# Optimization experiments

Hardware: AMD Instinct MI355X
Metric: run time of the kernel (lower is better)

Reference implementation:

```python
import jax, jax.numpy as jnp
import numpy as np

B, H, IN, OUT, T = 1024, 1024, 512, 8192, 15
EPS = 1e-5


def setup_inputs() -> dict:
    key = jax.random.key(0)
    ks = jax.random.split(key, 20)
    s = 0.02
    d = {
        'z': jax.random.normal(ks[0], (B, H), jnp.float32),
        'input_length': T,
        # ConvTranspose1d weights, torch layout [in, out, k] == jax 'IOH'
        'cw1': jax.random.normal(ks[1], (H, H, 3), jnp.float32) * s,
        'cb1': jax.random.normal(ks[2], (H,), jnp.float32) * s,
        'cw2': jax.random.normal(ks[3], (H, H, 3), jnp.float32) * s,
        'cb2': jax.random.normal(ks[4], (H,), jnp.float32) * s,
        'cw3': jax.random.normal(ks[5], (H, H, 3), jnp.float32) * s,
        'cb3': jax.random.normal(ks[6], (H,), jnp.float32) * s,
        # BatchNorm1d (eval mode: running stats)
        'bn1_g': jnp.ones((H,), jnp.float32), 'bn1_b': jnp.zeros((H,), jnp.float32),
        'bn1_m': jax.random.normal(ks[7], (H,), jnp.float32) * 0.1,
        'bn1_v': jax.random.uniform(ks[8], (H,), jnp.float32, 0.5, 1.5),
        'bn2_g': jnp.ones((H,), jnp.float32), 'bn2_b': jnp.zeros((H,), jnp.float32),
        'bn2_m': jax.random.normal(ks[9], (H,), jnp.float32) * 0.1,
        'bn2_v': jax.random.uniform(ks[10], (H,), jnp.float32, 0.5, 1.5),
        # GRUCell: weight_ih [3H, IN+H], weight_hh [3H, H]
        'w_ih': jax.random.normal(ks[11], (3 * H, IN + H), jnp.float32) * s,
        'w_hh': jax.random.normal(ks[12], (3 * H, H), jnp.float32) * s,
        'b_ih': jax.random.normal(ks[13], (3 * H,), jnp.float32) * s,
        'b_hh': jax.random.normal(ks[14], (3 * H,), jnp.float32) * s,
        # Linears (torch layout [out_features, in_features])
        'h2x_w': jax.random.normal(ks[15], (IN, H), jnp.float32) * s,
        'h2x_b': jax.random.normal(ks[16], (IN,), jnp.float32) * s,
        'dec2out_w': jax.random.normal(ks[17], (OUT, H), jnp.float32) * s,
        'dec2out_b': jnp.zeros((OUT,), jnp.float32),
        'out_w': jax.random.normal(ks[18], (OUT, H), jnp.float32) * s,
        'out_b': jnp.zeros((OUT,), jnp.float32),
    }
    return d


def _conv_t(x, w, b):
    # x: [B, C, L] ; torch ConvTranspose1d(k=3, s=2, pad=0): out L -> 2L+1
    y = jax.lax.conv_transpose(x, w, strides=(2,), padding='VALID',
                               dimension_numbers=('NCH', 'IOH', 'NCH'),
                               transpose_kernel=True)
    return y + b[None, :, None]


def _bn(x, g, bta, m, v):
    inv = g / jnp.sqrt(v + EPS)
    return (x - m[None, :, None]) * inv[None, :, None] + bta[None, :, None]


def reference(z, input_length, cw1, cb1, cw2, cb2, cw3, cb3,
              bn1_g, bn1_b, bn1_m, bn1_v, bn2_g, bn2_b, bn2_m, bn2_v,
              w_ih, w_hh, b_ih, b_hh, h2x_w, h2x_b,
              dec2out_w, dec2out_b, out_w, out_b):
    b = z.shape[0]
    # conv-transpose context: [B, H, 1] -> [B, H, 15]
    dec = z[:, :, None]
    dec = _bn(jax.nn.elu(_conv_t(dec, cw1, cb1)), bn1_g, bn1_b, bn1_m, bn1_v)
    dec = _bn(jax.nn.elu(_conv_t(dec, cw2, cb2)), bn2_g, bn2_b, bn2_m, bn2_v)
    dec = _conv_t(dec, cw3, cb3)
    dec_tbh = jnp.transpose(dec, (2, 0, 1))[:input_length]  # [T, B, H]

    inp0 = jnp.full((b, IN), float(OUT - 2), z.dtype)

    def step(carry, dec_t):
        h, inp = carry
        x = jnp.concatenate([inp, dec_t], axis=1)         # [B, IN+H]
        gi = x @ w_ih.T + b_ih
        gh = h @ w_hh.T + b_hh
        ir, iz, inn = jnp.split(gi, 3, axis=1)
        hr, hz, hn = jnp.split(gh, 3, axis=1)
        r = jax.nn.sigmoid(ir + hr)
        zg = jax.nn.sigmoid(iz + hz)
        n = jnp.tanh(inn + r * hn)
        h_new = (1.0 - zg) * n + zg * h
        inp_new = jax.nn.relu(h_new @ h2x_w.T + h2x_b)    # eval-mode branch
        return (h_new, inp_new), h_new

    (_, _), hs = jax.lax.scan(step, (z, inp0), dec_tbh)   # hs: [T, B, H]

    dec_flat = dec_tbh.reshape(-1, H)
    out_flat = hs.reshape(-1, H)
    dec_o = dec_flat @ dec2out_w.T + dec2out_b            # [T*B, OUT]
    output = out_flat @ out_w.T + out_b                   # [T*B, OUT]
    return output, dec_o
```

## Files before the change

kernel.cpp:

```cpp
#include <hip/hip_runtime.h>
#include <math.h>


#define HD    1024
#define BATCH 1024
#define IND   512
#define OUTD  8192
#define TSTEPS 15
#define EPSV  1e-5f

typedef unsigned short u16;
typedef __attribute__((ext_vector_type(8))) short bf16x8;
typedef __attribute__((ext_vector_type(8))) unsigned short u16x8;
typedef __attribute__((ext_vector_type(4))) unsigned short u16x4;
typedef __attribute__((ext_vector_type(4))) float f32x4;

__device__ __forceinline__ u16 f2b(float f) {
    union { float f; unsigned u; } x; x.f = f;
    unsigned r = x.u + 0x7fffu + ((x.u >> 16) & 1u);
    return (u16)(r >> 16);
}
__device__ __forceinline__ float b2f(u16 v) {
    union { unsigned u; float f; } x; x.u = ((unsigned)v) << 16; return x.f;
}

typedef __attribute__((address_space(1))) const void gas_t;
typedef __attribute__((address_space(3))) void las_t;
__device__ __forceinline__ void gload_lds16(const u16* g, u16* l) {
    __builtin_amdgcn_global_load_lds((gas_t*)g, (las_t*)l, 16, 0, 0);
}

template<int OUTB>
__launch_bounds__(512, 2)
__global__ void gemm256(int nbn, int nk,
    const u16* __restrict__ A, const u16* __restrict__ B,
    const float* __restrict__ bias, float* __restrict__ Cf,
    u16* __restrict__ Cb, int lda, int ldb, int ldc)
{
    const int nwg = gridDim.x;
    const int q = nwg >> 3, r = nwg & 7;
    const int xcd = blockIdx.x & 7, idx = blockIdx.x >> 3;
    const int wg = (xcd < r ? xcd * (q + 1) : r * (q + 1) + (xcd - r) * q) + idx;
    const int bm = (wg / nbn) * 256;
    const int bn = (wg % nbn) * 256;

    __shared__ __align__(16) u16 smem[2][2][256 * 64];
    u16 (*As)[256 * 64] = smem[0];
    u16 (*Bs)[256 * 64] = smem[1];

    const int tid = threadIdx.x;
    const int w = tid >> 6, l = tid & 63;
    const int wr = w >> 2, wc = w & 3;
    const int srow = l >> 3;
    const int scb  = (l & 7) ^ srow;
    const int fr = l & 15, fcb = l >> 4, swz = l & 7;

    const u16* Ag = A + (size_t)bm * lda;
    const u16* Bg = B + (size_t)bn * ldb;

    auto stage = [&](int b, int kt) {
        const int k0 = kt * 64 + scb * 8;
#pragma unroll
        for (int rr = 0; rr < 4; ++rr)
            gload_lds16(Ag + (size_t)(rr * 64 + w * 8 + srow) * lda + k0,
                        &As[b][(rr * 64 + w * 8) * 64]);
#pragma unroll
        for (int rr = 0; rr < 4; ++rr)
            gload_lds16(Bg + (size_t)(rr * 64 + w * 8 + srow) * ldb + k0,
                        &Bs[b][(rr * 64 + w * 8) * 64]);
    };

    f32x4 acc[8][4];
#pragma unroll
    for (int m = 0; m < 8; ++m)
#pragma unroll
        for (int n = 0; n < 4; ++n) acc[m][n] = (f32x4){0.f, 0.f, 0.f, 0.f};

    stage(0, 0);
    asm volatile("s_waitcnt vmcnt(0)" ::: "memory");
    asm volatile("s_barrier" ::: "memory");

    for (int kt = 0; kt < nk; ++kt) {
        const int c = kt & 1;
        if (kt + 1 < nk) stage(c ^ 1, kt + 1);
#pragma unroll
        for (int ks = 0; ks < 2; ++ks) {
            bf16x8 av[8], bv[4];
#pragma unroll
            for (int m = 0; m < 8; ++m)
                av[m] = *(const bf16x8*)&As[c][
                    (wr * 128 + m * 16 + fr) * 64 + (((ks * 4 + fcb) ^ swz) * 8)];
#pragma unroll
            for (int n = 0; n < 4; ++n)
                bv[n] = *(const bf16x8*)&Bs[c][
                    (wc * 64 + n * 16 + fr) * 64 + (((ks * 4 + fcb) ^ swz) * 8)];
            __builtin_amdgcn_s_setprio(1);
#pragma unroll
            for (int m = 0; m < 8; ++m)
#pragma unroll
                for (int n = 0; n < 4; ++n)
                    acc[m][n] = __builtin_amdgcn_mfma_f32_16x16x32_bf16(
                                    av[m], bv[n], acc[m][n], 0, 0, 0);
            __builtin_amdgcn_s_setprio(0);
        }
        asm volatile("s_waitcnt vmcnt(0)" ::: "memory");
        asm volatile("s_barrier" ::: "memory");
    }

    float* fsm = (float*)smem;
    const int row_h = (l >> 4) * 4;
#pragma unroll 1
    for (int hh = 0; hh < 2; ++hh) {
        __syncthreads();
        if (wr == hh) {
#pragma unroll
            for (int m = 0; m < 8; ++m)
#pragma unroll
                for (int j = 0; j < 4; ++j) {
                    const int rl = m * 16 + row_h + j;
#pragma unroll
                    for (int n = 0; n < 4; ++n)
                        fsm[rl * 256 + wc * 64 + n * 16 + fr] = acc[m][n][j];
                }
        }
        __syncthreads();
#pragma unroll
        for (int it = 0; it < 16; ++it) {
            const int fid = it * 512 + tid;
            const int rl = fid >> 6;
            const int cf = (fid & 63) * 4;
            float4 v = *(const float4*)&fsm[rl * 256 + cf];
            v.x += bias[bn + cf + 0];
            v.y += bias[bn + cf + 1];
            v.z += bias[bn + cf + 2];
            v.w += bias[bn + cf + 3];
            if (OUTB) {
                u16x4 o;
                o[0] = f2b(v.x); o[1] = f2b(v.y); o[2] = f2b(v.z); o[3] = f2b(v.w);
                *(u16x4*)&Cb[(size_t)(bm + hh * 128 + rl) * ldc + bn + cf] = o;
            } else {
                *(float4*)&Cf[(size_t)(bm + hh * 128 + rl) * ldc + bn + cf] = v;
            }
        }
    }
}

template<int EPI>
__device__ __forceinline__ void gemm_tile(
    int bm, int bn,
    int K1, const u16* A1, int lda1, const u16* B1, int ldb1,
    int K2, const u16* A2, int lda2, const u16* B2, int ldb2,
    const float* bias,
    const float* bng, const float* bnb, const float* bnm, const float* bnv,
    u16* Cb, int ldc)
{
    __shared__ __align__(16) u16 As[128 * 32];
    __shared__ __align__(16) u16 Bs[128 * 32];

    const int tid  = threadIdx.x;
    const int lane = tid & 63;
    const int w    = tid >> 6;
    const int wr   = w >> 1, wc = w & 1;
    const int r_in = lane >> 2;
    const int c_in = (lane & 3) * 8;

    f32x4 acc[4][4];
#pragma unroll
    for (int m = 0; m < 4; ++m)
#pragma unroll
        for (int n = 0; n < 4; ++n) acc[m][n] = (f32x4){0.f, 0.f, 0.f, 0.f};

#pragma unroll 1
    for (int pair = 0; pair < 2; ++pair) {
        const int K = pair ? K2 : K1;
        if (K == 0) continue;
        const int lda = pair ? lda2 : lda1;
        const int ldb = pair ? ldb2 : ldb1;
        const u16* Ag = (pair ? A2 : A1) + (size_t)bm * lda;
        const u16* Bg = (pair ? B2 : B1) + (size_t)bn * ldb;

        for (int k0 = 0; k0 < K; k0 += 32) {
#pragma unroll
            for (int i = 0; i < 2; ++i) {
                gload_lds16(Ag + (size_t)(i * 64 + w * 16 + r_in) * lda + k0 + c_in,
                            &As[i * 2048 + w * 512]);
                gload_lds16(Bg + (size_t)(i * 64 + w * 16 + r_in) * ldb + k0 + c_in,
                            &Bs[i * 2048 + w * 512]);
            }
            __syncthreads();

            const int fr = lane & 15;
            const int fk = (lane >> 4) * 8;
            bf16x8 av[4], bv[4];
#pragma unroll
            for (int m = 0; m < 4; ++m)
                av[m] = *(const bf16x8*)&As[(wr * 64 + m * 16 + fr) * 32 + fk];
#pragma unroll
            for (int n = 0; n < 4; ++n)
                bv[n] = *(const bf16x8*)&Bs[(wc * 64 + n * 16 + fr) * 32 + fk];
#pragma unroll
            for (int m = 0; m < 4; ++m)
#pragma unroll
                for (int n = 0; n < 4; ++n)
                    acc[m][n] = __builtin_amdgcn_mfma_f32_16x16x32_bf16(
                                    av[m], bv[n], acc[m][n], 0, 0, 0);
            __syncthreads();
        }
    }

    const int col_l = lane & 15;
    const int row_h = (lane >> 4) * 4;
#pragma unroll
    for (int m = 0; m < 4; ++m) {
#pragma unroll
        for (int j = 0; j < 4; ++j) {
            const int row = bm + wr * 64 + m * 16 + row_h + j;
#pragma unroll
            for (int n = 0; n < 4; ++n) {
                const int col = bn + wc * 64 + n * 16 + col_l;
                float v = acc[m][n][j] + bias[col];
                if (EPI == 1) {
                    float e = v > 0.f ? v : expm1f(v);
                    float sc = bng[col] * rsqrtf(bnv[col] + EPSV);
                    v = (e - bnm[col]) * sc + bnb[col];
                }
                Cb[(size_t)row * ldc + col] = f2b(v);
            }
        }
    }
}

template<int EPI>
__launch_bounds__(256)
__global__ void conv_gemm(int Lin, const u16* X, const u16* W, const float* bias,
                          const float* bng, const float* bnb, const float* bnm, const float* bnv,
                          u16* Y)
{
    const int t = blockIdx.z;
    int l0 = 0, k0 = 0, l1 = 0, k1 = 0, cnt = 0;
    for (int l = 0; l < Lin; ++l) {
        int k = t - 2 * l;
        if (k >= 0 && k < 3) { if (!cnt) { l0 = l; k0 = k; } else { l1 = l; k1 = k; } ++cnt; }
    }
    const size_t BH = (size_t)BATCH * HD, HH = (size_t)HD * HD;
    gemm_tile<EPI>(blockIdx.y * 128, blockIdx.x * 128,
        HD, X + l0 * BH, HD, W + k0 * HH, HD,
        cnt > 1 ? HD : 0, X + l1 * BH, HD, W + k1 * HH, HD,
        bias, bng, bnb, bnm, bnv, Y + (size_t)t * BH, HD);
}

#define KTILE(Ag, lda_, Bg, ldb_, k0_, ACC2)                                      \
  {                                                                               \
    const int k0 = (k0_);                                                         \
    gload_lds16((Ag) + (size_t)(tid >> 2) * (lda_) + k0 + (tid & 3) * 8,          \
                &As[tid * 8]);                                                    \
    _Pragma("unroll")                                                             \
    for (int i_ = 0; i_ < 3; ++i_) {                                              \
      const int u_ = tid + i_ * 256;                                              \
      gload_lds16((Bg) + (size_t)((u_ >> 8) * HD + bn + ((u_ & 255) >> 2)) * (ldb_)\
                       + k0 + (u_ & 3) * 8,                                       \
                  &Bs[u_ * 8]);                                                   \
    }                                                                             \
    __syncthreads();                                                              \
    {                                                                             \
      bf16x8 av0 = *(const bf16x8*)&As[(wr * 32 + fr) * 32 + fk];                 \
      bf16x8 av1 = *(const bf16x8*)&As[(wr * 32 + 16 + fr) * 32 + fk];            \
      _Pragma("unroll")                                                           \
      for (int n_ = 0; n_ < 2; ++n_) {                                            \
        const int bo = (wc * 32 + n_ * 16 + fr) * 32 + fk;                        \
        bf16x8 bv = *(const bf16x8*)&Bs[bo];                                      \
        ar[0][n_] = __builtin_amdgcn_mfma_f32_16x16x32_bf16(av0, bv, ar[0][n_], 0, 0, 0); \
        ar[1][n_] = __builtin_amdgcn_mfma_f32_16x16x32_bf16(av1, bv, ar[1][n_], 0, 0, 0); \
        bv = *(const bf16x8*)&Bs[2048 + bo];                                      \
        az[0][n_] = __builtin_amdgcn_mfma_f32_16x16x32_bf16(av0, bv, az[0][n_], 0, 0, 0); \
        az[1][n_] = __builtin_amdgcn_mfma_f32_16x16x32_bf16(av1, bv, az[1][n_], 0, 0, 0); \
        bv = *(const bf16x8*)&Bs[4096 + bo];                                      \
        ACC2[0][n_] = __builtin_amdgcn_mfma_f32_16x16x32_bf16(av0, bv, ACC2[0][n_], 0, 0, 0); \
        ACC2[1][n_] = __builtin_amdgcn_mfma_f32_16x16x32_bf16(av1, bv, ACC2[1][n_], 0, 0, 0); \
      }                                                                           \
    }                                                                             \
    __syncthreads();                                                              \
  }

__launch_bounds__(256)
__global__ void gih_cell(int t,
    const u16* __restrict__ inpb,  const u16* __restrict__ wih,
    const u16* __restrict__ hbp,   const u16* __restrict__ whh,
    const u16* __restrict__ gdect, const float* __restrict__ extra0,
    const float* __restrict__ b_hh, const float* __restrict__ hp,
    float* __restrict__ hf, u16* __restrict__ hsbt)
{
    const int bm = blockIdx.y * 64;
    const int bn = blockIdx.x * 64;
    __shared__ __align__(16) u16 As[64 * 32];
    __shared__ __align__(16) u16 Bs[3 * 64 * 32];

    const int tid = threadIdx.x, l = tid & 63, w = tid >> 6;
    const int wr = w >> 1, wc = w & 1;
    const int fr = l & 15, fk = (l >> 4) * 8;

    f32x4 ar[2][2], az[2][2], ain[2][2], ahn[2][2];
#pragma unroll
    for (int m = 0; m < 2; ++m)
#pragma unroll
        for (int n = 0; n < 2; ++n) {
            ar[m][n] = (f32x4){0.f, 0.f, 0.f, 0.f};
            az[m][n] = (f32x4){0.f, 0.f, 0.f, 0.f};
            ain[m][n] = (f32x4){0.f, 0.f, 0.f, 0.f};
            ahn[m][n] = (f32x4){0.f, 0.f, 0.f, 0.f};
        }

    const u16* Ah = hbp + (size_t)bm * HD;
    const u16* Ai = inpb + (size_t)bm * IND;
    for (int kt = 0; kt < 32; ++kt)
        KTILE(Ah, HD, whh, HD, kt * 32, ahn);
    if (t > 0)
        for (int kt = 0; kt < 16; ++kt)
            KTILE(Ai, IND, wih, (IND + HD), kt * 32, ain);

    const int rh = (l >> 4) * 4;
#pragma unroll
    for (int m = 0; m < 2; ++m)
#pragma unroll
        for (int n = 0; n < 2; ++n)
#pragma unroll
            for (int j = 0; j < 4; ++j) {
                const int R = bm + wr * 32 + m * 16 + rh + j;
                const int C = bn + wc * 32 + n * 16 + fr;
                const size_t g3 = (size_t)R * (3 * HD);
                float gr  = ar[m][n][j] + b2f(gdect[g3 + C])          + b_hh[C];
                float gz  = az[m][n][j] + b2f(gdect[g3 + HD + C])     + b_hh[HD + C];
                float gin = ain[m][n][j] + b2f(gdect[g3 + 2 * HD + C]);
                float ghn = ahn[m][n][j] + b_hh[2 * HD + C];
                if (extra0) {
                    gr  += extra0[C];
                    gz  += extra0[HD + C];
                    gin += extra0[2 * HD + C];
                }
                const float rg = 1.f / (1.f + expf(-gr));
                const float zg = 1.f / (1.f + expf(-gz));
                const float nn = tanhf(gin + rg * ghn);
                const float h  = (1.f - zg) * nn + zg * hp[(size_t)R * HD + C];
                hf[(size_t)R * HD + C] = h;
                hsbt[(size_t)R * HD + C] = f2b(h);
            }
}

__launch_bounds__(256)
__global__ void h2x_k(const u16* __restrict__ hbp, const u16* __restrict__ wx,
                      const float* __restrict__ xb, u16* __restrict__ inp)
{
    const int bm = blockIdx.y * 64;
    const int bn = blockIdx.x * 64;
    __shared__ __align__(16) u16 As[64 * 32];
    __shared__ __align__(16) u16 Bs[64 * 32];

    const int tid = threadIdx.x, l = tid & 63, w = tid >> 6;
    const int wr = w >> 1, wc = w & 1;
    const int fr = l & 15, fk = (l >> 4) * 8;

    f32x4 acc[2][2];
#pragma unroll
    for (int m = 0; m < 2; ++m)
#pragma unroll
        for (int n = 0; n < 2; ++n) acc[m][n] = (f32x4){0.f, 0.f, 0.f, 0.f};

    const u16* Ag = hbp + (size_t)bm * HD;
    const u16* Bg = wx + (size_t)bn * HD;
    for (int kt = 0; kt < 32; ++kt) {
        const int k0 = kt * 32;
        gload_lds16(Ag + (size_t)(tid >> 2) * HD + k0 + (tid & 3) * 8, &As[tid * 8]);
        gload_lds16(Bg + (size_t)(tid >> 2) * HD + k0 + (tid & 3) * 8, &Bs[tid * 8]);
        __syncthreads();
        bf16x8 av0 = *(const bf16x8*)&As[(wr * 32 + fr) * 32 + fk];
        bf16x8 av1 = *(const bf16x8*)&As[(wr * 32 + 16 + fr) * 32 + fk];
#pragma unroll
        for (int n = 0; n < 2; ++n) {
            bf16x8 bv = *(const bf16x8*)&Bs[(wc * 32 + n * 16 + fr) * 32 + fk];
            acc[0][n] = __builtin_amdgcn_mfma_f32_16x16x32_bf16(av0, bv, acc[0][n], 0, 0, 0);
            acc[1][n] = __builtin_amdgcn_mfma_f32_16x16x32_bf16(av1, bv, acc[1][n], 0, 0, 0);
        }
        __syncthreads();
    }
    const int rh = (l >> 4) * 4;
#pragma unroll
    for (int m = 0; m < 2; ++m)
#pragma unroll
        for (int n = 0; n < 2; ++n)
#pragma unroll
            for (int j = 0; j < 4; ++j) {
                const int R = bm + wr * 32 + m * 16 + rh + j;
                const int C = bn + wc * 32 + n * 16 + fr;
                inp[(size_t)R * IND + C] = f2b(fmaxf(acc[m][n][j] + xb[C], 0.f));
            }
}

__global__ void pack_w(const float* __restrict__ cw, u16* __restrict__ wp)
{
    __shared__ float lds[768];
    const int o = blockIdx.x, t = threadIdx.x;
    const float* src = cw + (size_t)o * (HD * 3);
    for (int i0 = 0; i0 < HD; i0 += 256) {
#pragma unroll
        for (int r = 0; r < 3; ++r) lds[t + 256 * r] = src[i0 * 3 + t + 256 * r];
        __syncthreads();
#pragma unroll
        for (int k = 0; k < 3; ++k)
            wp[(size_t)k * HD * HD + (size_t)o * HD + i0 + t] = f2b(lds[t * 3 + k]);
        __syncthreads();
    }
}

__global__ void f32_to_b16(const float* __restrict__ s, u16* __restrict__ d, int n)
{
    int i = (blockIdx.x * 256 + threadIdx.x) * 8;
    if (i >= n) return;
    float4 a = *(const float4*)(s + i);
    float4 b = *(const float4*)(s + i + 4);
    u16x8 o;
    o[0] = f2b(a.x); o[1] = f2b(a.y); o[2] = f2b(a.z); o[3] = f2b(a.w);
    o[4] = f2b(b.x); o[5] = f2b(b.y); o[6] = f2b(b.z); o[7] = f2b(b.w);
    *(u16x8*)(d + i) = o;
}

__global__ void ext0_k(const float* __restrict__ w_ih, float* __restrict__ e0)
{
    const int j = blockIdx.x, lane = threadIdx.x;
    float s = 0.f;
    for (int k = lane; k < IND; k += 64) s += w_ih[(size_t)j * (IND + HD) + k];
    for (int off = 32; off; off >>= 1) s += __shfl_down(s, off);
    if (lane == 0) e0[j] = 8190.f * s;
}

extern "C" void kernel_launch(void* const* d_in, const int* in_sizes, int n_in,
                              void* d_out, int out_size, void* d_ws, size_t ws_size,
                              hipStream_t stream)
{
    (void)in_sizes; (void)n_in; (void)out_size; (void)ws_size;

    const float* z    = (const float*)d_in[0];
    const float* cw1  = (const float*)d_in[2];
    const float* cb1  = (const float*)d_in[3];
    const float* cw2  = (const float*)d_in[4];
    const float* cb2  = (const float*)d_in[5];
    const float* cw3  = (const float*)d_in[6];
    const float* cb3  = (const float*)d_in[7];
    const float* bn1g = (const float*)d_in[8];
    const float* bn1b = (const float*)d_in[9];
    const float* bn1m = (const float*)d_in[10];
    const float* bn1v = (const float*)d_in[11];
    const float* bn2g = (const float*)d_in[12];
    const float* bn2b = (const float*)d_in[13];
    const float* bn2m = (const float*)d_in[14];
    const float* bn2v = (const float*)d_in[15];
    const float* w_ih = (const float*)d_in[16];
    const float* w_hh = (const float*)d_in[17];
    const float* b_ih = (const float*)d_in[18];
    const float* b_hh = (const float*)d_in[19];
    const float* h2xw = (const float*)d_in[20];
    const float* h2xb = (const float*)d_in[21];
    const float* d2ow = (const float*)d_in[22];
    const float* d2ob = (const float*)d_in[23];
    const float* outw = (const float*)d_in[24];
    const float* outb = (const float*)d_in[25];

    const size_t HH = (size_t)HD * HD, BH = (size_t)BATCH * HD;
    const size_t B3H = (size_t)BATCH * 3 * HD;

    u16* wsb = (u16*)d_ws;
    size_t off = 0;
    auto A16 = [&](size_t n) { u16* p = wsb + off; off += n; return p; };
    u16* wp1   = A16(3 * HH);
    u16* wp2   = A16(3 * HH);
    u16* wp3   = A16(3 * HH);
    u16* wihb  = A16((size_t)3 * HD * (IND + HD));
    u16* whhb  = A16(3 * HH);
    u16* h2xbw = A16((size_t)IND * HD);
    u16* outwb = A16((size_t)OUTD * HD);
    u16* d2owb = A16((size_t)OUTD * HD);
    u16* zb    = A16(BH);
    u16* decab = A16(3 * BH);
    u16* decbb = A16(7 * BH);
    u16* dec3b = A16(15 * BH);
    u16* hsb   = A16(15 * BH);
    u16* inpb  = A16((size_t)BATCH * IND);
    u16* gdecb = A16((size_t)TSTEPS * B3H);
    float* wsf = (float*)(wsb + ((off + 1) & ~(size_t)1));
    size_t foff = 0;
    auto A32 = [&](size_t n) { float* p = wsf + foff; foff += n; return p; };
    float* h0f   = A32(BH);
    float* h1f   = A32(BH);
    float* extra0= A32(3 * HD);

    pack_w<<<HD, 256, 0, stream>>>(cw1, wp1);
    pack_w<<<HD, 256, 0, stream>>>(cw2, wp2);
    pack_w<<<HD, 256, 0, stream>>>(cw3, wp3);
    auto cvt = [&](const float* s, u16* d, size_t n) {
        f32_to_b16<<<(unsigned)(n / 2048), 256, 0, stream>>>(s, d, (int)n);
    };
    cvt(z, zb, BH);
    cvt(w_ih, wihb, (size_t)3 * HD * (IND + HD));
    cvt(w_hh, whhb, 3 * HH);
    cvt(h2xw, h2xbw, (size_t)IND * HD);
    cvt(outw, outwb, (size_t)OUTD * HD);
    cvt(d2ow, d2owb, (size_t)OUTD * HD);
    ext0_k<<<3 * HD, 64, 0, stream>>>(w_ih, extra0);

    conv_gemm<1><<<dim3(8, 8, 3), 256, 0, stream>>>(1, zb, wp1, cb1,
        bn1g, bn1b, bn1m, bn1v, decab);
    conv_gemm<1><<<dim3(8, 8, 7), 256, 0, stream>>>(3, decab, wp2, cb2,
        bn2g, bn2b, bn2m, bn2v, decbb);
    conv_gemm<0><<<dim3(8, 8, 15), 256, 0, stream>>>(7, decbb, wp3, cb3,
        nullptr, nullptr, nullptr, nullptr, dec3b);

    gemm256<1><<<dim3((TSTEPS * BATCH / 256) * (3 * HD / 256)), 512, 0, stream>>>(
        3 * HD / 256, HD / 64,
        dec3b, wihb + IND, b_ih, nullptr, gdecb, HD, IND + HD, 3 * HD);

    for (int t = 0; t < TSTEPS; ++t) {
        const u16* hbp   = t ? hsb + (size_t)(t - 1) * BH : zb;
        const float* hpf = (t == 0) ? z : (((t - 1) & 1) ? h1f : h0f);
        float* hwf = (t & 1) ? h1f : h0f;
        if (t > 0)
            h2x_k<<<dim3(8, 16), 256, 0, stream>>>(hbp, h2xbw, h2xb, inpb);
        gih_cell<<<dim3(16, 16), 256, 0, stream>>>(t,
            inpb, wihb, hbp, whhb, gdecb + (size_t)t * B3H,
            t ? nullptr : extra0, b_hh, hpf, hwf, hsb + (size_t)t * BH);
    }

    float* out0 = (float*)d_out;
    float* out1 = out0 + (size_t)TSTEPS * BATCH * OUTD;
    const int nbn = OUTD / 256;
    const int nwg = (TSTEPS * BATCH / 256) * nbn;
    gemm256<0><<<dim3(nwg), 512, 0, stream>>>(nbn, HD / 64,
        hsb, outwb, outb, out0, nullptr, HD, HD, OUTD);
    gemm256<0><<<dim3(nwg), 512, 0, stream>>>(nbn, HD / 64,
        dec3b, d2owb, d2ob, out1, nullptr, HD, HD, OUTD);
}
```

Baseline: 1.668 ms.

## Fuse GRU recurrence into one cooperative kernel with grid syncs; swizzle GEMM tiles

Replaces the 29 per-timestep launches of h2x_k and gih_cell with a single cooperative kernel of 256 blocks. It loops over the 15 timesteps and uses grid-wide syncs between the h2x projection and the GRU cell update. This removes kernel launch gaps and tail effects in the serial recurrence, at the cost of grid barrier overhead and fixed occupancy. It also remaps gemm256 workgroups into 2x4 super-tiles to improve L2 reuse of the A and B tiles.

```diff
diff --git a/kernel.cpp b/kernel.cpp
--- a/kernel.cpp
+++ b/kernel.cpp
@@ -1,4 +1,5 @@
 #include <hip/hip_runtime.h>
+#include <hip/hip_cooperative_groups.h>
 #include <math.h>
 
 
@@ -41,8 +42,18 @@
     const int q = nwg >> 3, r = nwg & 7;
     const int xcd = blockIdx.x & 7, idx = blockIdx.x >> 3;
     const int wg = (xcd < r ? xcd * (q + 1) : r * (q + 1) + (xcd - r) * q) + idx;
-    const int bm = (wg / nbn) * 256;
-    const int bn = (wg % nbn) * 256;
+    int bm, bn;
+    const int nbm = nwg / nbn;
+    if ((nbn & 3) == 0 && (nbm & 1) == 0) {
+        const int nsc = nbn >> 2;
+        const int super = wg >> 3, inner = wg & 7;
+        const int sr = super / nsc, sc = super - sr * nsc;
+        bm = (sr * 2 + (inner >> 2)) * 256;
+        bn = (sc * 4 + (inner & 3)) * 256;
+    } else {
+        bm = (wg / nbn) * 256;
+        bn = (wg % nbn) * 256;
+    }
 
     __shared__ __align__(16) u16 smem[2][2][256 * 64];
     u16 (*As)[256 * 64] = smem[0];
@@ -283,116 +294,123 @@
   }
 
 __launch_bounds__(256)
-__global__ void gih_cell(int t,
-    const u16* __restrict__ inpb,  const u16* __restrict__ wih,
-    const u16* __restrict__ hbp,   const u16* __restrict__ whh,
-    const u16* __restrict__ gdect, const float* __restrict__ extra0,
-    const float* __restrict__ b_hh, const float* __restrict__ hp,
-    float* __restrict__ hf, u16* __restrict__ hsbt)
-{
-    const int bm = blockIdx.y * 64;
-    const int bn = blockIdx.x * 64;
+__global__ void gru_chain(
+    const u16* __restrict__ wih,  const u16* __restrict__ whh,
+    const u16* __restrict__ wx,   const float* __restrict__ xb,
+    const u16* __restrict__ gdecb, const float* __restrict__ extra0,
+    const float* __restrict__ b_hh,
+    const float* __restrict__ zf, const u16* __restrict__ zb,
+    u16* __restrict__ inpb, u16* __restrict__ hsb,
+    float* __restrict__ h0f, float* __restrict__ h1f)
+{
+    cooperative_groups::grid_group gg = cooperative_groups::this_grid();
+
     __shared__ __align__(16) u16 As[64 * 32];
     __shared__ __align__(16) u16 Bs[3 * 64 * 32];
 
+    const int bid = blockIdx.x;
     const int tid = threadIdx.x, l = tid & 63, w = tid >> 6;
     const int wr = w >> 1, wc = w & 1;
     const int fr = l & 15, fk = (l >> 4) * 8;
-
-    f32x4 ar[2][2], az[2][2], ain[2][2], ahn[2][2];
-#pragma unroll
-    for (int m = 0; m < 2; ++m)
-#pragma unroll
-        for (int n = 0; n < 2; ++n) {
-            ar[m][n] = (f32x4){0.f, 0.f, 0.f, 0.f};
-            az[m][n] = (f32x4){0.f, 0.f, 0.f, 0.f};
-            ain[m][n] = (f32x4){0.f, 0.f, 0.f, 0.f};
-            ahn[m][n] = (f32x4){0.f, 0.f, 0.f, 0.f};
-        }
-
-    const u16* Ah = hbp + (size_t)bm * HD;
-    const u16* Ai = inpb + (size_t)bm * IND;
-    for (int kt = 0; kt < 32; ++kt)
-        KTILE(Ah, HD, whh, HD, kt * 32, ahn);
-    if (t > 0)
-        for (int kt = 0; kt < 16; ++kt)
-            KTILE(Ai, IND, wih, (IND + HD), kt * 32, ain);
-
     const int rh = (l >> 4) * 4;
-#pragma unroll
-    for (int m = 0; m < 2; ++m)
-#pragma unroll
-        for (int n = 0; n < 2; ++n)
-#pragma unroll
-            for (int j = 0; j < 4; ++j) {
-                const int R = bm + wr * 32 + m * 16 + rh + j;
-                const int C = bn + wc * 32 + n * 16 + fr;
-                const size_t g3 = (size_t)R * (3 * HD);
-                float gr  = ar[m][n][j] + b2f(gdect[g3 + C])          + b_hh[C];
-                float gz  = az[m][n][j] + b2f(gdect[g3 + HD + C])     + b_hh[HD + C];
-                float gin = ain[m][n][j] + b2f(gdect[g3 + 2 * HD + C]);
-                float ghn = ahn[m][n][j] + b_hh[2 * HD + C];
-                if (extra0) {
-                    gr  += extra0[C];
-                    gz  += extra0[HD + C];
-                    gin += extra0[2 * HD + C];
+    const size_t BH = (size_t)BATCH * HD;
+    const size_t B3H = (size_t)BATCH * 3 * HD;
+
+    for (int t = 0; t < TSTEPS; ++t) {
+        const u16* hbp = t ? hsb + (size_t)(t - 1) * BH : zb;
+
+        if (t > 0 && bid < 128) {
+            const int bm = (bid >> 3) * 64;
+            const int bn = (bid & 7) * 64;
+            f32x4 acc[2][2];
+#pragma unroll
+            for (int m = 0; m < 2; ++m)
+#pragma unroll
+                for (int n = 0; n < 2; ++n) acc[m][n] = (f32x4){0.f, 0.f, 0.f, 0.f};
+            const u16* Ag = hbp + (size_t)bm * HD;
+            const u16* Bg = wx + (size_t)bn * HD;
+            for (int kt = 0; kt < 32; ++kt) {
+                const int k0 = kt * 32;
+                gload_lds16(Ag + (size_t)(tid >> 2) * HD + k0 + (tid & 3) * 8, &As[tid * 8]);
+                gload_lds16(Bg + (size_t)(tid >> 2) * HD + k0 + (tid & 3) * 8, &Bs[tid * 8]);
+                __syncthreads();
+                bf16x8 av0 = *(const bf16x8*)&As[(wr * 32 + fr) * 32 + fk];
+                bf16x8 av1 = *(const bf16x8*)&As[(wr * 32 + 16 + fr) * 32 + fk];
+#pragma unroll
+                for (int n = 0; n < 2; ++n) {
+                    bf16x8 bv = *(const bf16x8*)&Bs[(wc * 32 + n * 16 + fr) * 32 + fk];
+                    acc[0][n] = __builtin_amdgcn_mfma_f32_16x16x32_bf16(av0, bv, acc[0][n], 0, 0, 0);
+                    acc[1][n] = __builtin_amdgcn_mfma_f32_16x16x32_bf16(av1, bv, acc[1][n], 0, 0, 0);
                 }
-                const float rg = 1.f / (1.f + expf(-gr));
-                const float zg = 1.f / (1.f + expf(-gz));
-                const float nn = tanhf(gin + rg * ghn);
-                const float h  = (1.f - zg) * nn + zg * hp[(size_t)R * HD + C];
-                hf[(size_t)R * HD + C] = h;
-                hsbt[(size_t)R * HD + C] = f2b(h);
+                __syncthreads();
             }
-}
-
-__launch_bounds__(256)
-__global__ void h2x_k(const u16* __restrict__ hbp, const u16* __restrict__ wx,
-                      const float* __restrict__ xb, u16* __restrict__ inp)
-{
-    const int bm = blockIdx.y * 64;
-    const int bn = blockIdx.x * 64;
-    __shared__ __align__(16) u16 As[64 * 32];
-    __shared__ __align__(16) u16 Bs[64 * 32];
-
-    const int tid = threadIdx.x, l = tid & 63, w = tid >> 6;
-    const int wr = w >> 1, wc = w & 1;
-    const int fr = l & 15, fk = (l >> 4) * 8;
-
-    f32x4 acc[2][2];
-#pragma unroll
-    for (int m = 0; m < 2; ++m)
-#pragma unroll
-        for (int n = 0; n < 2; ++n) acc[m][n] = (f32x4){0.f, 0.f, 0.f, 0.f};
-
-    const u16* Ag = hbp + (size_t)bm * HD;
-    const u16* Bg = wx + (size_t)bn * HD;
-    for (int kt = 0; kt < 32; ++kt) {
-        const int k0 = kt * 32;
-        gload_lds16(Ag + (size_t)(tid >> 2) * HD + k0 + (tid & 3) * 8, &As[tid * 8]);
-        gload_lds16(Bg + (size_t)(tid >> 2) * HD + k0 + (tid & 3) * 8, &Bs[tid * 8]);
-        __syncthreads();
-        bf16x8 av0 = *(const bf16x8*)&As[(wr * 32 + fr) * 32 + fk];
-        bf16x8 av1 = *(const bf16x8*)&As[(wr * 32 + 16 + fr) * 32 + fk];
-#pragma unroll
-        for (int n = 0; n < 2; ++n) {
-            bf16x8 bv = *(const bf16x8*)&Bs[(wc * 32 + n * 16 + fr) * 32 + fk];
-            acc[0][n] = __builtin_amdgcn_mfma_f32_16x16x32_bf16(av0, bv, acc[0][n], 0, 0, 0);
-            acc[1][n] = __builtin_amdgcn_mfma_f32_16x16x32_bf16(av1, bv, acc[1][n], 0, 0, 0);
-        }
-        __syncthreads();
-    }
-    const int rh = (l >> 4) * 4;
-#pragma unroll
-    for (int m = 0; m < 2; ++m)
-#pragma unroll
-        for (int n = 0; n < 2; ++n)
-#pragma unroll
-            for (int j = 0; j < 4; ++j) {
-                const int R = bm + wr * 32 + m * 16 + rh + j;
-                const int C = bn + wc * 32 + n * 16 + fr;
-                inp[(size_t)R * IND + C] = f2b(fmaxf(acc[m][n][j] + xb[C], 0.f));
-            }
+#pragma unroll
+            for (int m = 0; m < 2; ++m)
+#pragma unroll
+                for (int n = 0; n < 2; ++n)
+#pragma unroll
+                    for (int j = 0; j < 4; ++j) {
+                        const int R = bm + wr * 32 + m * 16 + rh + j;
+                        const int C = bn + wc * 32 + n * 16 + fr;
+                        inpb[(size_t)R * IND + C] = f2b(fmaxf(acc[m][n][j] + xb[C], 0.f));
+                    }
+        }
+        gg.sync();
+
+        {
+            const int bm = (bid >> 4) * 64;
+            const int bn = (bid & 15) * 64;
+            f32x4 ar[2][2], az[2][2], ain[2][2], ahn[2][2];
+#pragma unroll
+            for (int m = 0; m < 2; ++m)
+#pragma unroll
+                for (int n = 0; n < 2; ++n) {
+                    ar[m][n] = (f32x4){0.f, 0.f, 0.f, 0.f};
+                    az[m][n] = (f32x4){0.f, 0.f, 0.f, 0.f};
+                    ain[m][n] = (f32x4){0.f, 0.f, 0.f, 0.f};
+                    ahn[m][n] = (f32x4){0.f, 0.f, 0.f, 0.f};
+                }
+            const u16* Ah = hbp + (size_t)bm * HD;
+            const u16* Ai = inpb + (size_t)bm * IND;
+            for (int kt = 0; kt < 32; ++kt)
+                KTILE(Ah, HD, whh, HD, kt * 32, ahn);
+            if (t > 0)
+                for (int kt = 0; kt < 16; ++kt)
+                    KTILE(Ai, IND, wih, (IND + HD), kt * 32, ain);
+
+            const u16* gdect = gdecb + (size_t)t * B3H;
+            const float* e0 = (t == 0) ? extra0 : nullptr;
+            const float* hp = (t == 0) ? zf : (((t - 1) & 1) ? h1f : h0f);
+            float* hw = (t & 1) ? h1f : h0f;
+            u16* hsbt = hsb + (size_t)t * BH;
+#pragma unroll
+            for (int m = 0; m < 2; ++m)
+#pragma unroll
+                for (int n = 0; n < 2; ++n)
+#pragma unroll
+                    for (int j = 0; j < 4; ++j) {
+                        const int R = bm + wr * 32 + m * 16 + rh + j;
+                        const int C = bn + wc * 32 + n * 16 + fr;
+                        const size_t g3 = (size_t)R * (3 * HD);
+                        float gr  = ar[m][n][j] + b2f(gdect[g3 + C])      + b_hh[C];
+                        float gz  = az[m][n][j] + b2f(gdect[g3 + HD + C]) + b_hh[HD + C];
+                        float gin = ain[m][n][j] + b2f(gdect[g3 + 2 * HD + C]);
+                        float ghn = ahn[m][n][j] + b_hh[2 * HD + C];
+                        if (e0) {
+                            gr  += e0[C];
+                            gz  += e0[HD + C];
+                            gin += e0[2 * HD + C];
+                        }
+                        const float rg = 1.f / (1.f + expf(-gr));
+                        const float zg = 1.f / (1.f + expf(-gz));
+                        const float nn = tanhf(gin + rg * ghn);
+                        const float h  = (1.f - zg) * nn + zg * hp[(size_t)R * HD + C];
+                        hw[(size_t)R * HD + C] = h;
+                        hsbt[(size_t)R * HD + C] = f2b(h);
+                    }
+        }
+        gg.sync();
+    }
 }
 
 __global__ void pack_w(const float* __restrict__ cw, u16* __restrict__ wp)
@@ -517,15 +535,15 @@
         3 * HD / 256, HD / 64,
         dec3b, wihb + IND, b_ih, nullptr, gdecb, HD, IND + HD, 3 * HD);
 
-    for (int t = 0; t < TSTEPS; ++t) {
-        const u16* hbp   = t ? hsb + (size_t)(t - 1) * BH : zb;
-        const float* hpf = (t == 0) ? z : (((t - 1) & 1) ? h1f : h0f);
-        float* hwf = (t & 1) ? h1f : h0f;
-        if (t > 0)
-            h2x_k<<<dim3(8, 16), 256, 0, stream>>>(hbp, h2xbw, h2xb, inpb);
-        gih_cell<<<dim3(16, 16), 256, 0, stream>>>(t,
-            inpb, wihb, hbp, whhb, gdecb + (size_t)t * B3H,
-            t ? nullptr : extra0, b_hh, hpf, hwf, hsb + (size_t)t * BH);
+    {
+        void* ka[] = {
+            (void*)&wihb, (void*)&whhb, (void*)&h2xbw, (void*)&h2xb,
+            (void*)&gdecb, (void*)&extra0, (void*)&b_hh,
+            (void*)&z, (void*)&zb, (void*)&inpb, (void*)&hsb,
+            (void*)&h0f, (void*)&h1f
+        };
+        hipLaunchCooperativeKernel((const void*)gru_chain,
+            dim3(256), dim3(256), ka, 0, stream);
     }
 
     float* out0 = (float*)d_out;
```

Measured after the change: 2.537 ms. +52.1%, slower.

## Overlap output projections with sequential GRU steps via rider blocks

Applied to the files above, without the earlier changes.

The two large output-projection GEMMs are split into 128x128 tiles. Those tiles are appended as extra 'rider' workgroups to the per-timestep h2x and GRU-cell launches, so idle CUs do projection work while the latency-bound recurrence runs. A final small launch covers the last timestep's hidden-state projection. The gemm256 kernel also gains a 2x4 supertile workgroup remapping for better cache locality. The riders use a simpler single-buffered 128-tile GEMM with scalar fp32 stores, which may be less efficient than the 256-tile kernel and may delay the recurrent critical path.

```diff
diff --git a/kernel.cpp b/kernel.cpp
--- a/kernel.cpp
+++ b/kernel.cpp
@@ -30,19 +30,142 @@
     __builtin_amdgcn_global_load_lds((gas_t*)g, (las_t*)l, 16, 0, 0);
 }
 
-template<int OUTB>
+template<int EPI, bool WF32, bool WB16>
+__device__ __forceinline__ void gemm_tile128(
+    u16* As, u16* Bs,
+    int bm, int bn,
+    int K1, const u16* A1, int lda1, const u16* B1, int ldb1,
+    int K2, const u16* A2, int lda2, const u16* B2, int ldb2,
+    const float* bias,
+    const float* bng, const float* bnb, const float* bnm, const float* bnv,
+    float* Cf, u16* Cb, int ldc)
+{
+    const int tid  = threadIdx.x;
+    const int lane = tid & 63;
+    const int w    = tid >> 6;
+    const int wr   = w >> 1, wc = w & 1;
+    const int r_in = lane >> 2;
+    const int c_in = (lane & 3) * 8;
+
+    f32x4 acc[4][4];
+#pragma unroll
+    for (int m = 0; m < 4; ++m)
+#pragma unroll
+        for (int n = 0; n < 4; ++n) acc[m][n] = (f32x4){0.f, 0.f, 0.f, 0.f};
+
+#pragma unroll 1
+    for (int pair = 0; pair < 2; ++pair) {
+        const int K = pair ? K2 : K1;
+        if (K == 0) continue;
+        const int lda = pair ? lda2 : lda1;
+        const int ldb = pair ? ldb2 : ldb1;
+        const u16* Ag = (pair ? A2 : A1) + (size_t)bm * lda;
+        const u16* Bg = (pair ? B2 : B1) + (size_t)bn * ldb;
+
+        for (int k0 = 0; k0 < K; k0 += 32) {
+#pragma unroll
+            for (int i = 0; i < 2; ++i) {
+                gload_lds16(Ag + (size_t)(i * 64 + w * 16 + r_in) * lda + k0 + c_in,
+                            &As[i * 2048 + w * 512]);
+                gload_lds16(Bg + (size_t)(i * 64 + w * 16 + r_in) * ldb + k0 + c_in,
+                            &Bs[i * 2048 + w * 512]);
+            }
+            __syncthreads();
+
+            const int fr = lane & 15;
+            const int fk = (lane >> 4) * 8;
+            bf16x8 av[4], bv[4];
+#pragma unroll
+            for (int m = 0; m < 4; ++m)
+                av[m] = *(const bf16x8*)&As[(wr * 64 + m * 16 + fr) * 32 + fk];
+#pragma unroll
+            for (int n = 0; n < 4; ++n)
+                bv[n] = *(const bf16x8*)&Bs[(wc * 64 + n * 16 + fr) * 32 + fk];
+#pragma unroll
+            for (int m = 0; m < 4; ++m)
+#pragma unroll
+                for (int n = 0; n < 4; ++n)
+                    acc[m][n] = __builtin_amdgcn_mfma_f32_16x16x32_bf16(
+                                    av[m], bv[n], acc[m][n], 0, 0, 0);
+            __syncthreads();
+        }
+    }
+
+    const int col_l = lane & 15;
+    const int row_h = (lane >> 4) * 4;
+#pragma unroll
+    for (int m = 0; m < 4; ++m) {
+#pragma unroll
+        for (int j = 0; j < 4; ++j) {
+            const int row = bm + wr * 64 + m * 16 + row_h + j;
+#pragma unroll
+            for (int n = 0; n < 4; ++n) {
+                const int col = bn + wc * 64 + n * 16 + col_l;
+                float v = acc[m][n][j] + bias[col];
+                if (EPI == 1) {
+                    float e = v > 0.f ? v : expm1f(v);
+                    float sc = bng[col] * rsqrtf(bnv[col] + EPSV);
+                    v = (e - bnm[col]) * sc + bnb[col];
+                }
+                if (WF32) Cf[(size_t)row * ldc + col] = v;
+                if (WB16) Cb[(size_t)row * ldc + col] = f2b(v);
+            }
+        }
+    }
+}
+
+__device__ __forceinline__ void proj_rider(u16* sm, int g,
+    const u16* A, const u16* B, const float* bias, float* C)
+{
+    gemm_tile128<0, true, false>(sm, sm + 4096,
+        (g >> 6) * 128, (g & 63) * 128,
+        HD, A, HD, B, HD, 0, nullptr, 0, nullptr, 0,
+        bias, nullptr, nullptr, nullptr, nullptr, C, nullptr, OUTD);
+}
+
+template<int EPI>
+__launch_bounds__(256)
+__global__ void conv_gemm(int Lin, const u16* X, const u16* W, const float* bias,
+                          const float* bng, const float* bnb, const float* bnm, const float* bnv,
+                          u16* Y)
+{
+    __shared__ __align__(16) u16 sm[8192];
+    const int t = blockIdx.z;
+    int l0 = 0, k0 = 0, l1 = 0, k1 = 0, cnt = 0;
+    for (int l = 0; l < Lin; ++l) {
+        int k = t - 2 * l;
+        if (k >= 0 && k < 3) { if (!cnt) { l0 = l; k0 = k; } else { l1 = l; k1 = k; } ++cnt; }
+    }
+    const size_t BH = (size_t)BATCH * HD, HH = (size_t)HD * HD;
+    gemm_tile128<EPI, false, true>(sm, sm + 4096,
+        blockIdx.y * 128, blockIdx.x * 128,
+        HD, X + l0 * BH, HD, W + k0 * HH, HD,
+        cnt > 1 ? HD : 0, X + l1 * BH, HD, W + k1 * HH, HD,
+        bias, bng, bnb, bnm, bnv, nullptr, Y + (size_t)t * BH, HD);
+}
+
 __launch_bounds__(512, 2)
 __global__ void gemm256(int nbn, int nk,
     const u16* __restrict__ A, const u16* __restrict__ B,
-    const float* __restrict__ bias, float* __restrict__ Cf,
-    u16* __restrict__ Cb, int lda, int ldb, int ldc)
+    const float* __restrict__ bias, u16* __restrict__ Cb,
+    int lda, int ldb, int ldc)
 {
     const int nwg = gridDim.x;
     const int q = nwg >> 3, r = nwg & 7;
     const int xcd = blockIdx.x & 7, idx = blockIdx.x >> 3;
     const int wg = (xcd < r ? xcd * (q + 1) : r * (q + 1) + (xcd - r) * q) + idx;
-    const int bm = (wg / nbn) * 256;
-    const int bn = (wg % nbn) * 256;
+    int bm, bn;
+    const int nbm = nwg / nbn;
+    if ((nbn & 3) == 0 && (nbm & 1) == 0) {
+        const int nsc = nbn >> 2;
+        const int super = wg >> 3, inner = wg & 7;
+        const int sr = super / nsc, sc = super - sr * nsc;
+        bm = (sr * 2 + (inner >> 2)) * 256;
+        bn = (sc * 4 + (inner & 3)) * 256;
+    } else {
+        bm = (wg / nbn) * 256;
+        bn = (wg % nbn) * 256;
+    }
 
     __shared__ __align__(16) u16 smem[2][2][256 * 64];
     u16 (*As)[256 * 64] = smem[0];
@@ -134,119 +257,11 @@
             v.y += bias[bn + cf + 1];
             v.z += bias[bn + cf + 2];
             v.w += bias[bn + cf + 3];
-            if (OUTB) {
-                u16x4 o;
-                o[0] = f2b(v.x); o[1] = f2b(v.y); o[2] = f2b(v.z); o[3] = f2b(v.w);
-                *(u16x4*)&Cb[(size_t)(bm + hh * 128 + rl) * ldc + bn + cf] = o;
-            } else {
-                *(float4*)&Cf[(size_t)(bm + hh * 128 + rl) * ldc + bn + cf] = v;
-            }
-        }
-    }
-}
-
-template<int EPI>
-__device__ __forceinline__ void gemm_tile(
-    int bm, int bn,
-    int K1, const u16* A1, int lda1, const u16* B1, int ldb1,
-    int K2, const u16* A2, int lda2, const u16* B2, int ldb2,
-    const float* bias,
-    const float* bng, const float* bnb, const float* bnm, const float* bnv,
-    u16* Cb, int ldc)
-{
-    __shared__ __align__(16) u16 As[128 * 32];
-    __shared__ __align__(16) u16 Bs[128 * 32];
-
-    const int tid  = threadIdx.x;
-    const int lane = tid & 63;
-    const int w    = tid >> 6;
-    const int wr   = w >> 1, wc = w & 1;
-    const int r_in = lane >> 2;
-    const int c_in = (lane & 3) * 8;
-
-    f32x4 acc[4][4];
-#pragma unroll
-    for (int m = 0; m < 4; ++m)
-#pragma unroll
-        for (int n = 0; n < 4; ++n) acc[m][n] = (f32x4){0.f, 0.f, 0.f, 0.f};
-
-#pragma unroll 1
-    for (int pair = 0; pair < 2; ++pair) {
-        const int K = pair ? K2 : K1;
-        if (K == 0) continue;
-        const int lda = pair ? lda2 : lda1;
-        const int ldb = pair ? ldb2 : ldb1;
-        const u16* Ag = (pair ? A2 : A1) + (size_t)bm * lda;
-        const u16* Bg = (pair ? B2 : B1) + (size_t)bn * ldb;
-
-        for (int k0 = 0; k0 < K; k0 += 32) {
-#pragma unroll
-            for (int i = 0; i < 2; ++i) {
-                gload_lds16(Ag + (size_t)(i * 64 + w * 16 + r_in) * lda + k0 + c_in,
-                            &As[i * 2048 + w * 512]);
-                gload_lds16(Bg + (size_t)(i * 64 + w * 16 + r_in) * ldb + k0 + c_in,
-                            &Bs[i * 2048 + w * 512]);
-            }
-            __syncthreads();
-
-            const int fr = lane & 15;
-            const int fk = (lane >> 4) * 8;
-            bf16x8 av[4], bv[4];
-#pragma unroll
-            for (int m = 0; m < 4; ++m)
-                av[m] = *(const bf16x8*)&As[(wr * 64 + m * 16 + fr) * 32 + fk];
-#pragma unroll
-            for (int n = 0; n < 4; ++n)
-                bv[n] = *(const bf16x8*)&Bs[(wc * 64 + n * 16 + fr) * 32 + fk];
-#pragma unroll
-            for (int m = 0; m < 4; ++m)
-#pragma unroll
-                for (int n = 0; n < 4; ++n)
-                    acc[m][n] = __builtin_amdgcn_mfma_f32_16x16x32_bf16(
-                                    av[m], bv[n], acc[m][n], 0, 0, 0);
-            __syncthreads();
-        }
-    }
-
-    const int col_l = lane & 15;
-    const int row_h = (lane >> 4) * 4;
-#pragma unroll
-    for (int m = 0; m < 4; ++m) {
-#pragma unroll
-        for (int j = 0; j < 4; ++j) {
-            const int row = bm + wr * 64 + m * 16 + row_h + j;
-#pragma unroll
-            for (int n = 0; n < 4; ++n) {
-                const int col = bn + wc * 64 + n * 16 + col_l;
-                float v = acc[m][n][j] + bias[col];
-                if (EPI == 1) {
-                    float e = v > 0.f ? v : expm1f(v);
-                    float sc = bng[col] * rsqrtf(bnv[col] + EPSV);
-                    v = (e - bnm[col]) * sc + bnb[col];
-                }
-                Cb[(size_t)row * ldc + col] = f2b(v);
-            }
-        }
-    }
-}
-
-template<int EPI>
-__launch_bounds__(256)
-__global__ void conv_gemm(int Lin, const u16* X, const u16* W, const float* bias,
-                          const float* bng, const float* bnb, const float* bnm, const float* bnv,
-                          u16* Y)
-{
-    const int t = blockIdx.z;
-    int l0 = 0, k0 = 0, l1 = 0, k1 = 0, cnt = 0;
-    for (int l = 0; l < Lin; ++l) {
-        int k = t - 2 * l;
-        if (k >= 0 && k < 3) { if (!cnt) { l0 = l; k0 = k; } else { l1 = l; k1 = k; } ++cnt; }
-    }
-    const size_t BH = (size_t)BATCH * HD, HH = (size_t)HD * HD;
-    gemm_tile<EPI>(blockIdx.y * 128, blockIdx.x * 128,
-        HD, X + l0 * BH, HD, W + k0 * HH, HD,
-        cnt > 1 ? HD : 0, X + l1 * BH, HD, W + k1 * HH, HD,
-        bias, bng, bnb, bnm, bnv, Y + (size_t)t * BH, HD);
+            u16x4 o;
+            o[0] = f2b(v.x); o[1] = f2b(v.y); o[2] = f2b(v.z); o[3] = f2b(v.w);
+            *(u16x4*)&Cb[(size_t)(bm + hh * 128 + rl) * ldc + bn + cf] = o;
+        }
+    }
 }
 
 #define KTILE(Ag, lda_, Bg, ldb_, k0_, ACC2)                                      \
@@ -288,16 +303,25 @@
     const u16* __restrict__ hbp,   const u16* __restrict__ whh,
     const u16* __restrict__ gdect, const float* __restrict__ extra0,
     const float* __restrict__ b_hh, const float* __restrict__ hp,
-    float* __restrict__ hf, u16* __restrict__ hsbt)
-{
-    const int bm = blockIdx.y * 64;
-    const int bn = blockIdx.x * 64;
-    __shared__ __align__(16) u16 As[64 * 32];
-    __shared__ __align__(16) u16 Bs[3 * 64 * 32];
-
+    float* __restrict__ hf, u16* __restrict__ hsbt,
+    const u16* __restrict__ dec3b, const u16* __restrict__ d2owb,
+    const float* __restrict__ d2ob, float* __restrict__ out1)
+{
+    __shared__ __align__(16) u16 sm[8192];
+    const int bid = blockIdx.x;
     const int tid = threadIdx.x, l = tid & 63, w = tid >> 6;
     const int wr = w >> 1, wc = w & 1;
     const int fr = l & 15, fk = (l >> 4) * 8;
+
+    if (bid >= 256) {
+        proj_rider(sm, t * 512 + (bid - 256), dec3b, d2owb, d2ob, out1);
+        return;
+    }
+
+    u16* As = sm;
+    u16* Bs = sm + 2048;
+    const int bm = (bid >> 4) * 64;
+    const int bn = (bid & 15) * 64;
 
     f32x4 ar[2][2], az[2][2], ain[2][2], ahn[2][2];
 #pragma unroll
@@ -328,8 +352,8 @@
                 const int R = bm + wr * 32 + m * 16 + rh + j;
                 const int C = bn + wc * 32 + n * 16 + fr;
                 const size_t g3 = (size_t)R * (3 * HD);
-                float gr  = ar[m][n][j] + b2f(gdect[g3 + C])          + b_hh[C];
-                float gz  = az[m][n][j] + b2f(gdect[g3 + HD + C])     + b_hh[HD + C];
+                float gr  = ar[m][n][j] + b2f(gdect[g3 + C])      + b_hh[C];
+                float gz  = az[m][n][j] + b2f(gdect[g3 + HD + C]) + b_hh[HD + C];
                 float gin = ain[m][n][j] + b2f(gdect[g3 + 2 * HD + C]);
                 float ghn = ahn[m][n][j] + b_hh[2 * HD + C];
                 if (extra0) {
@@ -347,24 +371,33 @@
 }
 
 __launch_bounds__(256)
-__global__ void h2x_k(const u16* __restrict__ hbp, const u16* __restrict__ wx,
-                      const float* __restrict__ xb, u16* __restrict__ inp)
-{
-    const int bm = blockIdx.y * 64;
-    const int bn = blockIdx.x * 64;
-    __shared__ __align__(16) u16 As[64 * 32];
-    __shared__ __align__(16) u16 Bs[64 * 32];
-
+__global__ void h2x_k(int t,
+    const u16* __restrict__ hbp, const u16* __restrict__ wx,
+    const float* __restrict__ xb, u16* __restrict__ inp,
+    const u16* __restrict__ hsb, const u16* __restrict__ outwb,
+    const float* __restrict__ outb, float* __restrict__ out0)
+{
+    __shared__ __align__(16) u16 sm[8192];
+    const int bid = blockIdx.x;
     const int tid = threadIdx.x, l = tid & 63, w = tid >> 6;
     const int wr = w >> 1, wc = w & 1;
     const int fr = l & 15, fk = (l >> 4) * 8;
 
+    if (bid >= 128) {
+        proj_rider(sm, (t - 1) * 512 + (bid - 128), hsb, outwb, outb, out0);
+        return;
+    }
+
+    u16* As = sm;
+    u16* Bs = sm + 2048;
+    const int bm = (bid >> 3) * 64;
+    const int bn = (bid & 7) * 64;
+
     f32x4 acc[2][2];
 #pragma unroll
     for (int m = 0; m < 2; ++m)
 #pragma unroll
         for (int n = 0; n < 2; ++n) acc[m][n] = (f32x4){0.f, 0.f, 0.f, 0.f};
-
     const u16* Ag = hbp + (size_t)bm * HD;
     const u16* Bg = wx + (size_t)bn * HD;
     for (int kt = 0; kt < 32; ++kt) {
@@ -393,6 +426,14 @@
                 const int C = bn + wc * 32 + n * 16 + fr;
                 inp[(size_t)R * IND + C] = f2b(fmaxf(acc[m][n][j] + xb[C], 0.f));
             }
+}
+
+__launch_bounds__(256)
+__global__ void proj_k(int g0, const u16* __restrict__ A, const u16* __restrict__ B,
+                       const float* __restrict__ bias, float* __restrict__ C)
+{
+    __shared__ __align__(16) u16 sm[8192];
+    proj_rider(sm, g0 + blockIdx.x, A, B, bias, C);
 }
 
 __global__ void pack_w(const float* __restrict__ cw, u16* __restrict__ wp)
@@ -513,27 +554,23 @@
     conv_gemm<0><<<dim3(8, 8, 15), 256, 0, stream>>>(7, decbb, wp3, cb3,
         nullptr, nullptr, nullptr, nullptr, dec3b);
 
-    gemm256<1><<<dim3((TSTEPS * BATCH / 256) * (3 * HD / 256)), 512, 0, stream>>>(
+    gemm256<<<dim3((TSTEPS * BATCH / 256) * (3 * HD / 256)), 512, 0, stream>>>(
         3 * HD / 256, HD / 64,
-        dec3b, wihb + IND, b_ih, nullptr, gdecb, HD, IND + HD, 3 * HD);
-
+        dec3b, wihb + IND, b_ih, gdecb, HD, IND + HD, 3 * HD);
+
+    float* out0 = (float*)d_out;
+    float* out1 = out0 + (size_t)TSTEPS * BATCH * OUTD;
     for (int t = 0; t < TSTEPS; ++t) {
         const u16* hbp   = t ? hsb + (size_t)(t - 1) * BH : zb;
         const float* hpf = (t == 0) ? z : (((t - 1) & 1) ? h1f : h0f);
         float* hwf = (t & 1) ? h1f : h0f;
         if (t > 0)
-            h2x_k<<<dim3(8, 16), 256, 0, stream>>>(hbp, h2xbw, h2xb, inpb);
-        gih_cell<<<dim3(16, 16), 256, 0, stream>>>(t,
+            h2x_k<<<640, 256, 0, stream>>>(t, hbp, h2xbw, h2xb, inpb,
+                hsb, outwb, outb, out0);
+        gih_cell<<<768, 256, 0, stream>>>(t,
             inpb, wihb, hbp, whhb, gdecb + (size_t)t * B3H,
-            t ? nullptr : extra0, b_hh, hpf, hwf, hsb + (size_t)t * BH);
-    }
-
-    float* out0 = (float*)d_out;
-    float* out1 = out0 + (size_t)TSTEPS * BATCH * OUTD;
-    const int nbn = OUTD / 256;
-    const int nwg = (TSTEPS * BATCH / 256) * nbn;
-    gemm256<0><<<dim3(nwg), 512, 0, stream>>>(nbn, HD / 64,
-        hsb, outwb, outb, out0, nullptr, HD, HD, OUTD);
-    gemm256<0><<<dim3(nwg), 512, 0, stream>>>(nbn, HD / 64,
-        dec3b, d2owb, d2ob, out1, nullptr, HD, HD, OUTD);
-}
+            t ? nullptr : extra0, b_hh, hpf, hwf, hsb + (size_t)t * BH,
+            dec3b, d2owb, d2ob, out1);
+    }
+    proj_k<<<512, 256, 0, stream>>>(14 * 512, hsb, outwb, outb, out0);
+}
```

Result: faster. 1.537 ms (-7.8%).
